# Optimization experiments

Measured on AMD Instinct MI355X. Metric: run time of the kernel, lower is better.

Reference implementation:

```python
import jax, jax.numpy as jnp
import numpy as np

B, N, N2 = 4, 4096, 4096
CIN, DIM, KNN, UP = 128, 64, 20, 2
HPOS, HATT = 64, 256
EPS = 1e-5


def _group(feat, idx):
    # feat: (B,C,M), idx: (B,N,K) -> (B,C,N,K) gather of neighbor features
    return jax.vmap(lambda f, i: f[:, i])(feat, idx)


def _conv1d(w, b, x):
    # 1x1 Conv1d: w (O,C), x (B,C,N)
    return jnp.einsum('oc,bcn->bon', w, x) + b[:, None]


def _bn(x, g, be, m, v):
    # eval-mode BatchNorm2d on (B,C,N,K)
    inv = g / jnp.sqrt(v + EPS)
    return x * inv[:, None, None] + (be - m * inv)[:, None, None]


def setup_inputs() -> dict:
    key = jax.random.key(0)
    ks = jax.random.split(key, 32)
    r = lambda i, s: jax.random.normal(ks[i], s, jnp.float32)
    u = lambda i, s: jax.random.uniform(ks[i], s, jnp.float32, 0.5, 1.5)
    return {
        'pos1': r(0, (B, 3, N)),
        'query': r(1, (B, CIN, N)),
        'pos2': r(2, (B, 3, N2)),
        'key_feat': r(3, (B, CIN, N2)),
        'wq': r(4, (DIM, CIN)) * 0.05, 'bq': r(5, (DIM,)) * 0.05,
        'wk': r(6, (DIM, CIN)) * 0.05, 'bk': r(7, (DIM,)) * 0.05,
        'wv': r(8, (DIM, CIN)) * 0.05, 'bv': r(9, (DIM,)) * 0.05,
        'pw1': r(10, (HPOS, 3)) * 0.2, 'pb1': r(11, (HPOS,)) * 0.05,
        'pg': u(12, (HPOS,)), 'pbt': r(13, (HPOS,)) * 0.05,
        'pm': r(14, (HPOS,)) * 0.05, 'pv': u(15, (HPOS,)),
        'pw2': r(16, (DIM, HPOS)) * 0.1, 'pb2': r(17, (DIM,)) * 0.05,
        'aw1': r(18, (HATT, DIM)) * 0.1, 'ab1': r(19, (HATT,)) * 0.05,
        'ag': u(20, (HATT,)), 'abt2': r(21, (HATT,)) * 0.05,
        'am': r(22, (HATT,)) * 0.05, 'av': u(23, (HATT,)),
        'awt': r(24, (HATT, DIM, UP)) * 0.05, 'abt': r(25, (DIM,)) * 0.05,
        'we': r(26, (CIN, DIM)) * 0.1, 'be': r(27, (CIN,)) * 0.05,
    }


def reference(pos1, query, pos2, key_feat, wq, bq, wk, bk, wv, bv,
              pw1, pb1, pg, pbt, pm, pv, pw2, pb2,
              aw1, ab1, ag, abt2, am, av, awt, abt, we, be):
    q = _conv1d(wq, bq, query)          # (B,DIM,N)
    k = _conv1d(wk, bk, key_feat)       # (B,DIM,N2)
    v = _conv1d(wv, bv, key_feat)       # (B,DIM,N2)
    # KNN of pos1 queries into pos2 support set
    p1 = pos1.transpose(0, 2, 1)        # (B,N,3)
    p2 = pos2.transpose(0, 2, 1)        # (B,N2,3)
    d = (jnp.sum(p1 * p1, -1)[:, :, None] + jnp.sum(p2 * p2, -1)[:, None, :]
         - 2.0 * jnp.einsum('bnd,bmd->bnm', p1, p2))
    _, idx = jax.lax.top_k(-d, KNN)     # (B,N,KNN)
    kg = _group(k, idx)                 # (B,DIM,N,K)
    qk_rel = q[:, :, :, None] - kg
    pos_rel = pos1[:, :, :, None] - _group(pos2, idx)   # (B,3,N,K)
    # pos_mlp: conv2d 3->HPOS, BN, ReLU, conv2d HPOS->DIM
    pe = jnp.einsum('oc,bcnk->bonk', pw1, pos_rel) + pb1[:, None, None]
    pe = jax.nn.relu(_bn(pe, pg, pbt, pm, pv))
    pe = jnp.einsum('oc,bcnk->bonk', pw2, pe) + pb2[:, None, None]  # (B,DIM,N,K)
    # attn_mlp: conv2d DIM->HATT, BN, ReLU, ConvTranspose2d HATT->DIM kernel (UP,1)
    h = qk_rel + pe
    a = jnp.einsum('oc,bcnk->bonk', aw1, h) + ab1[:, None, None]
    a = jax.nn.relu(_bn(a, ag, abt2, am, av))               # (B,HATT,N,K)
    att = jnp.einsum('bcnk,cor->bonrk', a, awt).reshape(B, DIM, N * UP, KNN)
    att = att + abt[:, None, None]
    att = jax.nn.softmax(att, axis=-1)
    vg = _group(v, idx) + pe            # (B,DIM,N,K)
    vu = jnp.repeat(vg, UP, axis=2)     # nearest upsample -> (B,DIM,N*UP,K)
    agg = jnp.sum(att * vu, axis=-1)    # (B,DIM,N*UP)
    y = _conv1d(we, be, agg)            # (B,CIN,N*UP)
    identity = jnp.repeat(query, UP, axis=2)  # residual (in==out -> Identity)
    return y + identity
```

## Files before the change

kernel.cpp:

```cpp
#include <hip/hip_runtime.h>
#include <hip/hip_bf16.h>

#define BATCH 4
#define NPTS  4096
#define NPTS2 4096
#define CIN   128
#define DIM   64
#define KNN   20
#define UPF   2
#define HPOS  64
#define HATT  256
#define MOUT  8192
#define EPSF  1e-5f
#define QPB   3
#define BPB   1366

#define FB_KNN   1024
#define FB_PKV   (FB_KNN + 256)
#define FB_PQ    (FB_PKV + 256)
#define FB_PACK  (FB_PQ + 128)

typedef _Float16 h16x8 __attribute__((ext_vector_type(8)));
typedef _Float16 h16x4 __attribute__((ext_vector_type(4)));
typedef _Float16 h16x2 __attribute__((ext_vector_type(2)));
typedef float    f32x4 __attribute__((ext_vector_type(4)));

__device__ inline float rdlane(float v, int src) {
  return __int_as_float(__builtin_amdgcn_readlane(__float_as_int(v), src));
}

__device__ __forceinline__ float distf(float qn, float m2x, float m2y, float m2z,
                                       float x, float y, float z) {
  float s = __fmaf_rn(x, x, qn);
  s = __fmaf_rn(y, y, s);
  s = __fmaf_rn(z, z, s);
  s = __fmaf_rn(m2x, x, s);
  s = __fmaf_rn(m2y, y, s);
  s = __fmaf_rn(m2z, z, s);
  return s;
}

__global__ __launch_bounds__(256) void front(
    const float* __restrict__ pos1, const float* __restrict__ pos2,
    int* __restrict__ idxout,
    const float* __restrict__ key_feat,
    const float* __restrict__ wk, const float* __restrict__ bk,
    const float* __restrict__ wv, const float* __restrict__ bv,
    float* __restrict__ k_t, float* __restrict__ v_t,
    const float* __restrict__ query,
    const float* __restrict__ wq, const float* __restrict__ bq,
    float* __restrict__ q_t,
    const float* __restrict__ aw1, const float* __restrict__ awt,
    const float* __restrict__ pw2,
    const float* __restrict__ ag,  const float* __restrict__ av,
    const float* __restrict__ abt2, const float* __restrict__ am,
    const float* __restrict__ abt,
    const float* __restrict__ pg,  const float* __restrict__ pv,
    const float* __restrict__ pbt, const float* __restrict__ pm,
    const float* __restrict__ ab1, const float* __restrict__ pb1,
    const float* __restrict__ pw1,
    _Float16* __restrict__ aw1h, _Float16* __restrict__ awtP,
    _Float16* __restrict__ pw2h, float* __restrict__ abtX,
    float* __restrict__ ab1f, float* __restrict__ pw1f,
    float* __restrict__ pb1f) {
  __shared__ union {
    struct { float X[CIN][64]; float O[64][65]; } pj;
    struct { int cnt[16]; float dbuf[16][64]; int jbuf[16][64]; } kn;
  } smU;
  const int bid = blockIdx.x;
  const int t   = threadIdx.x;

  if (bid < FB_KNN) {
    const int lane = t & 63;
    const int wv   = t >> 6;
    const int b    = bid >> 8;
    const int nb   = (bid & 255) * 16;
    const float* p2x = pos2 + (b * 3 + 0) * NPTS2;
    const float* p2y = pos2 + (b * 3 + 1) * NPTS2;
    const float* p2z = pos2 + (b * 3 + 2) * NPTS2;

    float qn[4], m2x[4], m2y[4], m2z[4];
#pragma unroll
    for (int qi = 0; qi < 4; ++qi) {
      int n = nb + wv * 4 + qi;
      float qx = pos1[(b * 3 + 0) * NPTS + n];
      float qy = pos1[(b * 3 + 1) * NPTS + n];
      float qz = pos1[(b * 3 + 2) * NPTS + n];
      qn[qi]  = qx * qx + qy * qy + qz * qz;
      m2x[qi] = -2.0f * qx; m2y[qi] = -2.0f * qy; m2z[qi] = -2.0f * qz;
    }

    float mymin[4] = {3.402823466e38f, 3.402823466e38f,
                      3.402823466e38f, 3.402823466e38f};
    f32x4 cx[4], cy[4], cz[4];
#pragma unroll 1
    for (int c = 0; c < 4; ++c) {
      int base = c * 1024 + lane * 4;
#pragma unroll
      for (int g = 0; g < 4; ++g) {
        cx[g] = *(const f32x4*)(p2x + base + g * 256);
        cy[g] = *(const f32x4*)(p2y + base + g * 256);
        cz[g] = *(const f32x4*)(p2z + base + g * 256);
      }
#pragma unroll
      for (int qi = 0; qi < 4; ++qi)
#pragma unroll
        for (int g = 0; g < 4; ++g)
#pragma unroll
          for (int e = 0; e < 4; ++e) {
            float d = distf(qn[qi], m2x[qi], m2y[qi], m2z[qi],
                            cx[g][e], cy[g][e], cz[g][e]);
            mymin[qi] = fminf(mymin[qi], d);
          }
    }

    float T0[4];
#pragma unroll
    for (int qi = 0; qi < 4; ++qi) {
      float v = mymin[qi];
#pragma unroll
      for (int k = 2; k <= 64; k <<= 1)
#pragma unroll
        for (int jj = k >> 1; jj >= 1; jj >>= 1) {
          float o = __shfl_xor(v, jj);
          bool up = ((lane & k) == 0);
          bool keepmin = (((lane & jj) == 0) == up);
          v = keepmin ? fminf(v, o) : fmaxf(v, o);
        }
      T0[qi] = rdlane(v, 19);
    }

    if (lane < 4) smU.kn.cnt[wv * 4 + lane] = 0;

#pragma unroll 1
    for (int c = 0; c < 4; ++c) {
      int base = c * 1024 + lane * 4;
#pragma unroll
      for (int g = 0; g < 4; ++g) {
        cx[g] = *(const f32x4*)(p2x + base + g * 256);
        cy[g] = *(const f32x4*)(p2y + base + g * 256);
        cz[g] = *(const f32x4*)(p2z + base + g * 256);
      }
#pragma unroll
      for (int qi = 0; qi < 4; ++qi) {
        const int qq = wv * 4 + qi;
#pragma unroll
        for (int g = 0; g < 4; ++g)
#pragma unroll
          for (int e = 0; e < 4; ++e) {
            float d = distf(qn[qi], m2x[qi], m2y[qi], m2z[qi],
                            cx[g][e], cy[g][e], cz[g][e]);
            if (d <= T0[qi]) {
              int slot = atomicAdd(&smU.kn.cnt[qq], 1);
              if (slot < 64) { smU.kn.dbuf[qq][slot] = d; smU.kn.jbuf[qq][slot] = base + g * 256 + e; }
            }
          }
      }
    }

#pragma unroll 1
    for (int qi = 0; qi < 4; ++qi) {
      const int qq = wv * 4 + qi;
      const int n  = nb + qq;
      const int cnt = smU.kn.cnt[qq];
      if (cnt <= 64) {
        float dk = (lane < cnt) ? smU.kn.dbuf[qq][lane] : 3.402823466e38f;
        int   jk = (lane < cnt) ? smU.kn.jbuf[qq][lane] : 0x7fffffff;
#pragma unroll
        for (int k = 2; k <= 64; k <<= 1) {
#pragma unroll
          for (int jj = k >> 1; jj >= 1; jj >>= 1) {
            float od = __shfl_xor(dk, jj);
            int   oj = __shfl_xor(jk, jj);
            bool mineSm = (dk < od) || (dk == od && jk < oj);
            bool up = ((lane & k) == 0);
            bool keepmin = (((lane & jj) == 0) == up);
            bool takeOther = (keepmin != mineSm);
            dk = takeOther ? od : dk;
            jk = takeOther ? oj : jk;
          }
        }
        if (lane < KNN) idxout[(b * NPTS + n) * KNN + lane] = jk;
      } else {
        float dl = 3.402823466e38f;
        int   il = 0;
        for (int j0 = 0; j0 < NPTS2; j0 += 64) {
          int j = j0 + lane;
          float d = distf(qn[qi], m2x[qi], m2y[qi], m2z[qi], p2x[j], p2y[j], p2z[j]);
          float T = rdlane(dl, 19);
          unsigned long long m = __ballot(d < T);
          while (m) {
            int src = __ffsll(m) - 1;
            m &= m - 1;
            float dd = rdlane(d, src);
            float T2 = rdlane(dl, 19);
            if (dd < T2) {
              int jj2 = j0 + src;
              float pd = __shfl_up(dl, 1);
              int   pi = __shfl_up(il, 1);
              if (dl > dd) {
                if (lane == 0 || pd <= dd) { dl = dd; il = jj2; }
                else                       { dl = pd; il = pi; }
              }
            }
          }
        }
        if (lane < KNN) idxout[(b * NPTS + n) * KNN + lane] = il;
      }
    }
  } else if (bid < FB_PKV) {
    const int vb = bid - FB_KNN;
    const int b  = vb >> 6;
    const int n0 = (vb & 63) * 64;
    for (int l = t; l < CIN * 64; l += 256) {
      int c = l >> 6, i = l & 63;
      smU.pj.X[c][i] = key_feat[(b * CIN + c) * NPTS2 + n0 + i];
    }
    __syncthreads();
    const int n_l = t & 63;
    const int w   = __builtin_amdgcn_readfirstlane(t >> 6);
    float acck[16], accv[16];
#pragma unroll
    for (int i = 0; i < 16; ++i) { acck[i] = bk[w * 16 + i]; accv[i] = bv[w * 16 + i]; }
    for (int c = 0; c < CIN; ++c) {
      float xv = smU.pj.X[c][n_l];
#pragma unroll
      for (int i = 0; i < 16; ++i) {
        acck[i] += wk[(w * 16 + i) * CIN + c] * xv;
        accv[i] += wv[(w * 16 + i) * CIN + c] * xv;
      }
    }
#pragma unroll
    for (int i = 0; i < 16; ++i) smU.pj.O[n_l][w * 16 + i] = acck[i];
    __syncthreads();
    for (int l = t; l < 64 * 64; l += 256)
      k_t[(b * NPTS2 + n0 + (l >> 6)) * DIM + (l & 63)] = smU.pj.O[l >> 6][l & 63];
    __syncthreads();
#pragma unroll
    for (int i = 0; i < 16; ++i) smU.pj.O[n_l][w * 16 + i] = accv[i];
    __syncthreads();
    for (int l = t; l < 64 * 64; l += 256)
      v_t[(b * NPTS2 + n0 + (l >> 6)) * DIM + (l & 63)] = smU.pj.O[l >> 6][l & 63];
  } else if (bid < FB_PQ) {
    const int vb = bid - FB_PKV;
    const int b  = vb >> 6;
    const int n0 = (vb & 63) * 64;
    for (int l = t; l < CIN * 64; l += 256) {
      int c = l >> 6, i = l & 63;
      smU.pj.X[c][i] = query[(b * CIN + c) * NPTS + n0 + i];
    }
    __syncthreads();
    const int n_l = t & 63;
    const int w   = __builtin_amdgcn_readfirstlane(t >> 6);
    float acc[16];
#pragma unroll
    for (int i = 0; i < 16; ++i) acc[i] = bq[w * 16 + i];
    for (int c = 0; c < CIN; ++c) {
      float xv = smU.pj.X[c][n_l];
#pragma unroll
      for (int i = 0; i < 16; ++i) acc[i] += wq[(w * 16 + i) * CIN + c] * xv;
    }
#pragma unroll
    for (int i = 0; i < 16; ++i) smU.pj.O[n_l][w * 16 + i] = acc[i];
    __syncthreads();
    for (int l = t; l < 64 * 64; l += 256)
      q_t[(b * NPTS + n0 + (l >> 6)) * DIM + (l & 63)] = smU.pj.O[l >> 6][l & 63];
  } else {
    int i = (bid - FB_PQ) * 256 + t;
    if (i < 16384) {
      int j = i >> 6;
      float inv = ag[j] / sqrtf(av[j] + EPSF);
      aw1h[i] = (_Float16)(aw1[i] * inv);
    }
    if (i < 32768) {
      int orr = i >> 8, j = i & 255;
      awtP[i] = (_Float16)awt[j * 128 + orr];
    }
    if (i < 4096) pw2h[i] = (_Float16)pw2[i];
    if (i < 256) {
      float inv = ag[i] / sqrtf(av[i] + EPSF);
      ab1f[i] = ab1[i] * inv + (abt2[i] - am[i] * inv);
    }
    if (i < 192) {
      int hc = i / 3;
      float inv = pg[hc] / sqrtf(pv[hc] + EPSF);
      pw1f[i] = pw1[i] * inv;
    }
    if (i < 128) abtX[i] = abt[i >> 1];
    if (i < 64) {
      float inv = pg[i] / sqrtf(pv[i] + EPSF);
      pb1f[i] = pb1[i] * inv + (pbt[i] - pm[i] * inv);
    }
  }
}

#define SM_R0    0
#define SM_R1    9216
#define SM_LGC   0
#define SM_VGB   18432

__global__ __launch_bounds__(256, 4) void attn_mfma(
    const float* __restrict__ q_t, const float* __restrict__ k_t,
    const float* __restrict__ v_t, const int* __restrict__ idx,
    const float* __restrict__ pos1, const float* __restrict__ pos2,
    const float* __restrict__ pw1f, const float* __restrict__ pb1f,
    const _Float16* __restrict__ pw2h, const float* __restrict__ pb2,
    const _Float16* __restrict__ aw1h, const float* __restrict__ ab1f,
    const _Float16* __restrict__ awtP, const float* __restrict__ abtX,
    float* __restrict__ agg) {
  __shared__ __align__(16) char smem[27136];
  const int b  = blockIdx.x / BPB;
  const int n0 = (blockIdx.x - b * BPB) * QPB;
  const int t  = threadIdx.x;
  const int lane = t & 63;
  const int w  = t >> 6;
  const int r  = lane & 15;
  const int q4 = lane >> 4;

  const int colB = t & 63, cgB = t >> 6;
  const int pB = colB / 20, kkB = colB - pB * 20;
  const bool okB = (pB < QPB) && (n0 + pB < NPTS);
  const int nqB = okB ? (n0 + pB) : 0;
  int jB = 0;
  if (okB) jB = idx[(b * NPTS + nqB) * KNN + kkB];

  f32x4 qk4[4], vv4[4];
  {
    const float* qrow = q_t + ((size_t)(b * NPTS  + nqB)) * DIM + cgB * 16;
    const float* krow = k_t + ((size_t)(b * NPTS2 + jB))  * DIM + cgB * 16;
    const float* vrow = v_t + ((size_t)(b * NPTS2 + jB))  * DIM + cgB * 16;
#pragma unroll
    for (int u = 0; u < 4; ++u) {
      f32x4 qv = *(const f32x4*)(qrow + u * 4);
      f32x4 kv = *(const f32x4*)(krow + u * 4);
      qk4[u] = qv - kv;
      vv4[u] = *(const f32x4*)(vrow + u * 4);
    }
  }

  {
    float p0 = 0.f, p1 = 0.f, p2 = 0.f;
    if (okB) {
      p0 = pos1[(b * 3 + 0) * NPTS + nqB] - pos2[(b * 3 + 0) * NPTS2 + jB];
      p1 = pos1[(b * 3 + 1) * NPTS + nqB] - pos2[(b * 3 + 1) * NPTS2 + jB];
      p2 = pos1[(b * 3 + 2) * NPTS + nqB] - pos2[(b * 3 + 2) * NPTS2 + jB];
    }
#pragma unroll
    for (int hf = 0; hf < 2; ++hf) {
      h16x8 pk;
#pragma unroll
      for (int ii = 0; ii < 8; ++ii) {
        int hc = cgB * 16 + hf * 8 + ii;
        float v0 = pb1f[hc] + pw1f[hc*3] * p0 + pw1f[hc*3+1] * p1 + pw1f[hc*3+2] * p2;
        v0 = fmaxf(v0, 0.f);
        if (!okB) v0 = 0.f;
        pk[ii] = (_Float16)v0;
      }
      *(h16x8*)(smem + SM_R0 + ((colB * 72 + cgB * 16 + hf * 8) * 2)) = pk;
    }
  }
  __syncthreads();

  {
    h16x8 a0[2];
#pragma unroll
    for (int ks = 0; ks < 2; ++ks)
      a0[ks] = *(const h16x8*)&pw2h[(w * 16 + r) * 64 + ks * 32 + q4 * 8];
    f32x4 acc[4];
#pragma unroll
    for (int nt = 0; nt < 4; ++nt) acc[nt] = (f32x4){0.f, 0.f, 0.f, 0.f};
#pragma unroll
    for (int ks = 0; ks < 2; ++ks)
#pragma unroll
      for (int nt = 0; nt < 4; ++nt) {
        h16x8 bv = *(h16x8*)(smem + SM_R0 + ((nt * 16 + r) * 72 + ks * 32 + q4 * 8) * 2);
        acc[nt] = __builtin_amdgcn_mfma_f32_16x16x32_f16(a0[ks], bv, acc[nt], 0, 0, 0);
      }
    int o0 = w * 16 + q4 * 4;
    f32x4 pbv = *(const f32x4*)&pb2[o0];
#pragma unroll
    for (int nt = 0; nt < 4; ++nt) {
      f32x4 vv = acc[nt] + pbv;
      h16x4 pk = {(_Float16)vv[0], (_Float16)vv[1], (_Float16)vv[2], (_Float16)vv[3]};
      *(h16x4*)(smem + SM_R1 + ((nt * 16 + r) * 72 + o0) * 2) = pk;
    }
  }

  {
    h16x8 pe8[2];
#pragma unroll
    for (int hf = 0; hf < 2; ++hf)
      pe8[hf] = *(h16x8*)(smem + SM_R1 + (colB * 72 + cgB * 16 + hf * 8) * 2);
    h16x8 hp8[2];
#pragma unroll
    for (int u = 0; u < 4; ++u) {
      int hf = u >> 1, e0 = (u & 1) * 4;
      f32x4 pe = {(float)pe8[hf][e0],     (float)pe8[hf][e0 + 1],
                  (float)pe8[hf][e0 + 2], (float)pe8[hf][e0 + 3]};
      f32x4 hv = qk4[u] + pe;
      f32x4 gv = vv4[u] + pe;
      if (!okB) { hv = (f32x4){0.f,0.f,0.f,0.f}; gv = hv; }
      hp8[hf][e0]     = (_Float16)hv[0];
      hp8[hf][e0 + 1] = (_Float16)hv[1];
      hp8[hf][e0 + 2] = (_Float16)hv[2];
      hp8[hf][e0 + 3] = (_Float16)hv[3];
      h16x4 gp = {(_Float16)gv[0], (_Float16)gv[1], (_Float16)gv[2], (_Float16)gv[3]};
      *(h16x4*)(smem + SM_VGB + (colB * 68 + cgB * 16 + u * 4) * 2) = gp;
    }
#pragma unroll
    for (int hf = 0; hf < 2; ++hf)
      *(h16x8*)(smem + SM_R1 + (colB * 72 + cgB * 16 + hf * 8) * 2) = hp8[hf];
  }
  __syncthreads();

  h16x8 bs[2][4];
#pragma unroll
  for (int ks = 0; ks < 2; ++ks)
#pragma unroll
    for (int nt = 0; nt < 4; ++nt)
      bs[ks][nt] = *(h16x8*)(smem + SM_R1 + ((nt * 16 + r) * 72 + ks * 32 + q4 * 8) * 2);

  f32x4 accD[2][4];
#pragma unroll
  for (int h = 0; h < 2; ++h)
#pragma unroll
    for (int nt = 0; nt < 4; ++nt) accD[h][nt] = (f32x4){0.f, 0.f, 0.f, 0.f};

#define C_QUARTER(quar, base)                                                  \
  {                                                                            \
    int mt = (quar) * 4 + w;                                                   \
    h16x8 af0 = *(const h16x8*)&aw1h[(mt * 16 + r) * 64 + q4 * 8];             \
    h16x8 af1 = *(const h16x8*)&aw1h[(mt * 16 + r) * 64 + 32 + q4 * 8];        \
    f32x4 acc[4];                                                              \
    _Pragma("unroll")                                                          \
    for (int nt = 0; nt < 4; ++nt) acc[nt] = (f32x4){0.f, 0.f, 0.f, 0.f};      \
    _Pragma("unroll")                                                          \
    for (int nt = 0; nt < 4; ++nt)                                             \
      acc[nt] = __builtin_amdgcn_mfma_f32_16x16x32_f16(af0, bs[0][nt], acc[nt], 0, 0, 0); \
    _Pragma("unroll")                                                          \
    for (int nt = 0; nt < 4; ++nt)                                             \
      acc[nt] = __builtin_amdgcn_mfma_f32_16x16x32_f16(af1, bs[1][nt], acc[nt], 0, 0, 0); \
    int j0  = mt * 16 + q4 * 4;                                                \
    int jq0 = j0 - (quar) * 64;                                                \
    f32x4 b1 = *(const f32x4*)&ab1f[j0];                                       \
    _Pragma("unroll")                                                          \
    for (int nt = 0; nt < 4; ++nt) {                                           \
      int col = nt * 16 + r;                                                   \
      float v0 = fmaxf(acc[nt][0] + b1[0], 0.f);                               \
      float v1 = fmaxf(acc[nt][1] + b1[1], 0.f);                               \
      float v2 = fmaxf(acc[nt][2] + b1[2], 0.f);                               \
      float v3 = fmaxf(acc[nt][3] + b1[3], 0.f);                               \
      h16x4 pk = {(_Float16)v0, (_Float16)v1, (_Float16)v2, (_Float16)v3};     \
      *(h16x4*)(smem + (base) + (col * 72 + jq0) * 2) = pk;                    \
    }                                                                          \
  }

#define D_QUARTER(quar, base)                                                  \
  {                                                                            \
    _Pragma("unroll")                                                          \
    for (int ks2 = 0; ks2 < 2; ++ks2) {                                        \
      h16x8 bsv[4];                                                            \
      _Pragma("unroll")                                                        \
      for (int nt = 0; nt < 4; ++nt)                                           \
        bsv[nt] = *(h16x8*)(smem + (base) + ((nt * 16 + r) * 72 + ks2 * 32 + q4 * 8) * 2); \
      int ksg = (quar) * 2 + ks2;                                              \
      _Pragma("unroll")                                                        \
      for (int h = 0; h < 2; ++h) {                                            \
        int mt2 = w * 2 + h;                                                   \
        h16x8 af = *(const h16x8*)&awtP[(mt2 * 16 + r) * 256 + ksg * 32 + q4 * 8]; \
        _Pragma("unroll")                                                      \
        for (int nt = 0; nt < 4; ++nt)                                         \
          accD[h][nt] = __builtin_amdgcn_mfma_f32_16x16x32_f16(af, bsv[nt], accD[h][nt], 0, 0, 0); \
      }                                                                        \
    }                                                                          \
  }

  C_QUARTER(0, SM_R0)
  __syncthreads();
  D_QUARTER(0, SM_R0)
  C_QUARTER(1, SM_R1)
  __syncthreads();
  D_QUARTER(1, SM_R1)
  C_QUARTER(2, SM_R0)
  __syncthreads();
  D_QUARTER(2, SM_R0)
  C_QUARTER(3, SM_R1)
  __syncthreads();
  D_QUARTER(3, SM_R1)
  __syncthreads();

  {
#pragma unroll
    for (int h = 0; h < 2; ++h) {
      int orr0 = (w * 2 + h) * 16 + q4 * 4;
      f32x4 ab = *(const f32x4*)&abtX[orr0];
#pragma unroll
      for (int nt = 0; nt < 4; ++nt) {
        int col = nt * 16 + r;
        if (col < QPB * KNN) {
          f32x4 vv = accD[h][nt] + ab;
          h16x4 pk = {(_Float16)vv[0], (_Float16)vv[1], (_Float16)vv[2], (_Float16)vv[3]};
          *(h16x4*)(smem + SM_LGC + (col * 136 + orr0) * 2) = pk;
        }
      }
    }
  }
  __syncthreads();

  if (t < 64 * QPB) {
    int li = t & 63, p = t >> 6;
    if (n0 + p < NPTS) {
      h16x2 Lp[KNN];
      float G[KNN];
#pragma unroll
      for (int kk = 0; kk < KNN; ++kk) {
        Lp[kk] = *(h16x2*)(smem + SM_LGC + ((p * 20 + kk) * 136 + li * 2) * 2);
        G[kk]  = (float)*(_Float16*)(smem + SM_VGB + ((p * 20 + kk) * 68 + li) * 2);
      }
#pragma unroll
      for (int half = 0; half < 2; ++half) {
        float mx = (float)Lp[0][half];
#pragma unroll
        for (int kk = 1; kk < KNN; ++kk) mx = fmaxf(mx, (float)Lp[kk][half]);
        float s = 0.f, a = 0.f;
#pragma unroll
        for (int kk = 0; kk < KNN; ++kk) {
          float e = __expf((float)Lp[kk][half] - mx);
          s += e;
          a += e * G[kk];
        }
        float rs = 1.0f / s;
        agg[(((size_t)(b * NPTS + n0 + p)) * UPF + half) * DIM + li] = a * rs;
      }
    }
  }
#undef C_QUARTER
#undef D_QUARTER
}

__global__ __launch_bounds__(256) void out_proj(const float* __restrict__ agg,
    const float* __restrict__ we, const float* __restrict__ be,
    const float* __restrict__ query, float* __restrict__ out) {
  __shared__ float A[64][65];
  const int b  = blockIdx.x >> 7;
  const int m0 = (blockIdx.x & 127) * 64;
  const int t  = threadIdx.x;
  for (int l = t; l < 64 * 64; l += 256) {
    int row = l >> 6, c = l & 63;
    A[row][c] = agg[(b * MOUT + m0 + row) * DIM + c];
  }
  __syncthreads();
  const int m_l = t & 63;
  const int w   = __builtin_amdgcn_readfirstlane(t >> 6);
  float acc[32];
#pragma unroll
  for (int i = 0; i < 32; ++i) acc[i] = 0.f;
  for (int c = 0; c < DIM; ++c) {
    float a = A[m_l][c];
#pragma unroll
    for (int i = 0; i < 32; ++i) acc[i] += we[(w * 32 + i) * DIM + c] * a;
  }
  const int m = m0 + m_l;
#pragma unroll
  for (int i = 0; i < 32; ++i) {
    int o = w * 32 + i;
    out[(b * CIN + o) * MOUT + m] = acc[i] + be[o] + query[(b * CIN + o) * NPTS + (m >> 1)];
  }
}

extern "C" void kernel_launch(void* const* d_in, const int* in_sizes, int n_in,
                              void* d_out, int out_size, void* d_ws, size_t ws_size,
                              hipStream_t stream) {
  (void)in_sizes; (void)n_in; (void)out_size; (void)ws_size;
  const float* pos1     = (const float*)d_in[0];
  const float* query    = (const float*)d_in[1];
  const float* pos2     = (const float*)d_in[2];
  const float* key_feat = (const float*)d_in[3];
  const float* wq  = (const float*)d_in[4];
  const float* bq  = (const float*)d_in[5];
  const float* wk  = (const float*)d_in[6];
  const float* bk  = (const float*)d_in[7];
  const float* wv  = (const float*)d_in[8];
  const float* bv  = (const float*)d_in[9];
  const float* pw1 = (const float*)d_in[10];
  const float* pb1 = (const float*)d_in[11];
  const float* pg  = (const float*)d_in[12];
  const float* pbt = (const float*)d_in[13];
  const float* pm  = (const float*)d_in[14];
  const float* pv  = (const float*)d_in[15];
  const float* pw2 = (const float*)d_in[16];
  const float* pb2 = (const float*)d_in[17];
  const float* aw1 = (const float*)d_in[18];
  const float* ab1 = (const float*)d_in[19];
  const float* ag  = (const float*)d_in[20];
  const float* abt2= (const float*)d_in[21];
  const float* am  = (const float*)d_in[22];
  const float* av  = (const float*)d_in[23];
  const float* awt = (const float*)d_in[24];
  const float* abt = (const float*)d_in[25];
  const float* we  = (const float*)d_in[26];
  const float* be  = (const float*)d_in[27];

  float* ws   = (float*)d_ws;
  float* q_t  = ws;
  float* k_t  = q_t + BATCH * NPTS * DIM;
  float* v_t  = k_t + BATCH * NPTS2 * DIM;
  float* aggb = v_t + BATCH * NPTS2 * DIM;
  int*   idxb = (int*)(aggb + BATCH * MOUT * DIM);
  _Float16* aw1h = (_Float16*)(idxb + BATCH * NPTS * KNN);
  _Float16* awtP = aw1h + HATT * DIM;
  _Float16* pw2h = awtP + 128 * HATT;
  float* abtX    = (float*)(pw2h + DIM * HPOS);
  float* ab1f    = abtX + 128;
  float* pw1f    = ab1f + HATT;
  float* pb1f    = pw1f + HPOS * 3;

  front<<<FB_PACK, 256, 0, stream>>>(
      pos1, pos2, idxb,
      key_feat, wk, bk, wv, bv, k_t, v_t,
      query, wq, bq, q_t,
      aw1, awt, pw2, ag, av, abt2, am, abt,
      pg, pv, pbt, pm, ab1, pb1, pw1,
      aw1h, awtP, pw2h, abtX, ab1f, pw1f, pb1f);
  attn_mfma<<<BATCH * BPB, 256, 0, stream>>>(q_t, k_t, v_t, idxb, pos1, pos2,
      pw1f, pb1f, pw2h, pb2, aw1h, ab1f, awtP, abtX, aggb);
  out_proj<<<BATCH * (MOUT / 64), 256, 0, stream>>>(aggb, we, be, query, (float*)d_out);
}
```

Before: 318.4 us.

## Cut register pressure in attention MFMA kernel to raise occupancy to 5 blocks

Stops keeping the B fragments of the hidden tile and the preloaded A fragments in registers; they are now reloaded from shared memory inside each K-step. The C/D quarter stages drop the SM_R0/SM_R1 ping-pong, since SM_R1 now holds the persistent input, and use a single buffer with an extra barrier between stages. Launch bounds go from 4 to 5 blocks per SIMD-group so more waves can be resident. The trade is more LDS reads and twice the barriers in exchange for lower VGPR use and higher occupancy.

```diff
diff --git a/kernel.cpp b/kernel.cpp
--- a/kernel.cpp
+++ b/kernel.cpp
@@ -299,7 +299,7 @@
 #define SM_LGC   0
 #define SM_VGB   18432
 
-__global__ __launch_bounds__(256, 4) void attn_mfma(
+__global__ __launch_bounds__(256, 5) void attn_mfma(
     const float* __restrict__ q_t, const float* __restrict__ k_t,
     const float* __restrict__ v_t, const int* __restrict__ idx,
     const float* __restrict__ pos1, const float* __restrict__ pos2,
@@ -362,20 +362,18 @@
   __syncthreads();
 
   {
-    h16x8 a0[2];
-#pragma unroll
-    for (int ks = 0; ks < 2; ++ks)
-      a0[ks] = *(const h16x8*)&pw2h[(w * 16 + r) * 64 + ks * 32 + q4 * 8];
     f32x4 acc[4];
 #pragma unroll
     for (int nt = 0; nt < 4; ++nt) acc[nt] = (f32x4){0.f, 0.f, 0.f, 0.f};
 #pragma unroll
-    for (int ks = 0; ks < 2; ++ks)
+    for (int ks = 0; ks < 2; ++ks) {
+      h16x8 a0 = *(const h16x8*)&pw2h[(w * 16 + r) * 64 + ks * 32 + q4 * 8];
 #pragma unroll
       for (int nt = 0; nt < 4; ++nt) {
         h16x8 bv = *(h16x8*)(smem + SM_R0 + ((nt * 16 + r) * 72 + ks * 32 + q4 * 8) * 2);
-        acc[nt] = __builtin_amdgcn_mfma_f32_16x16x32_f16(a0[ks], bv, acc[nt], 0, 0, 0);
-      }
+        acc[nt] = __builtin_amdgcn_mfma_f32_16x16x32_f16(a0, bv, acc[nt], 0, 0, 0);
+      }
+    }
     int o0 = w * 16 + q4 * 4;
     f32x4 pbv = *(const f32x4*)&pb2[o0];
 #pragma unroll
@@ -413,33 +411,29 @@
   }
   __syncthreads();
 
-  h16x8 bs[2][4];
-#pragma unroll
-  for (int ks = 0; ks < 2; ++ks)
-#pragma unroll
-    for (int nt = 0; nt < 4; ++nt)
-      bs[ks][nt] = *(h16x8*)(smem + SM_R1 + ((nt * 16 + r) * 72 + ks * 32 + q4 * 8) * 2);
-
   f32x4 accD[2][4];
 #pragma unroll
   for (int h = 0; h < 2; ++h)
 #pragma unroll
     for (int nt = 0; nt < 4; ++nt) accD[h][nt] = (f32x4){0.f, 0.f, 0.f, 0.f};
 
-#define C_QUARTER(quar, base)                                                  \
+#define C_QUARTER(quar)                                                        \
   {                                                                            \
     int mt = (quar) * 4 + w;                                                   \
-    h16x8 af0 = *(const h16x8*)&aw1h[(mt * 16 + r) * 64 + q4 * 8];             \
-    h16x8 af1 = *(const h16x8*)&aw1h[(mt * 16 + r) * 64 + 32 + q4 * 8];        \
     f32x4 acc[4];                                                              \
     _Pragma("unroll")                                                          \
     for (int nt = 0; nt < 4; ++nt) acc[nt] = (f32x4){0.f, 0.f, 0.f, 0.f};      \
     _Pragma("unroll")                                                          \
-    for (int nt = 0; nt < 4; ++nt)                                             \
-      acc[nt] = __builtin_amdgcn_mfma_f32_16x16x32_f16(af0, bs[0][nt], acc[nt], 0, 0, 0); \
-    _Pragma("unroll")                                                          \
-    for (int nt = 0; nt < 4; ++nt)                                             \
-      acc[nt] = __builtin_amdgcn_mfma_f32_16x16x32_f16(af1, bs[1][nt], acc[nt], 0, 0, 0); \
+    for (int ks = 0; ks < 2; ++ks) {                                           \
+      h16x8 af = *(const h16x8*)&aw1h[(mt * 16 + r) * 64 + ks * 32 + q4 * 8];  \
+      h16x8 bsv[4];                                                            \
+      _Pragma("unroll")                                                        \
+      for (int nt = 0; nt < 4; ++nt)                                           \
+        bsv[nt] = *(h16x8*)(smem + SM_R1 + ((nt * 16 + r) * 72 + ks * 32 + q4 * 8) * 2); \
+      _Pragma("unroll")                                                        \
+      for (int nt = 0; nt < 4; ++nt)                                           \
+        acc[nt] = __builtin_amdgcn_mfma_f32_16x16x32_f16(af, bsv[nt], acc[nt], 0, 0, 0); \
+    }                                                                          \
     int j0  = mt * 16 + q4 * 4;                                                \
     int jq0 = j0 - (quar) * 64;                                                \
     f32x4 b1 = *(const f32x4*)&ab1f[j0];                                       \
@@ -451,18 +445,18 @@
       float v2 = fmaxf(acc[nt][2] + b1[2], 0.f);                               \
       float v3 = fmaxf(acc[nt][3] + b1[3], 0.f);                               \
       h16x4 pk = {(_Float16)v0, (_Float16)v1, (_Float16)v2, (_Float16)v3};     \
-      *(h16x4*)(smem + (base) + (col * 72 + jq0) * 2) = pk;                    \
+      *(h16x4*)(smem + SM_R0 + (col * 72 + jq0) * 2) = pk;                     \
     }                                                                          \
   }
 
-#define D_QUARTER(quar, base)                                                  \
+#define D_QUARTER(quar)                                                        \
   {                                                                            \
     _Pragma("unroll")                                                          \
     for (int ks2 = 0; ks2 < 2; ++ks2) {                                        \
       h16x8 bsv[4];                                                            \
       _Pragma("unroll")                                                        \
       for (int nt = 0; nt < 4; ++nt)                                           \
-        bsv[nt] = *(h16x8*)(smem + (base) + ((nt * 16 + r) * 72 + ks2 * 32 + q4 * 8) * 2); \
+        bsv[nt] = *(h16x8*)(smem + SM_R0 + ((nt * 16 + r) * 72 + ks2 * 32 + q4 * 8) * 2); \
       int ksg = (quar) * 2 + ks2;                                              \
       _Pragma("unroll")                                                        \
       for (int h = 0; h < 2; ++h) {                                            \
@@ -475,18 +469,21 @@
     }                                                                          \
   }
 
-  C_QUARTER(0, SM_R0)
-  __syncthreads();
-  D_QUARTER(0, SM_R0)
-  C_QUARTER(1, SM_R1)
-  __syncthreads();
-  D_QUARTER(1, SM_R1)
-  C_QUARTER(2, SM_R0)
-  __syncthreads();
-  D_QUARTER(2, SM_R0)
-  C_QUARTER(3, SM_R1)
-  __syncthreads();
-  D_QUARTER(3, SM_R1)
+  C_QUARTER(0)
+  __syncthreads();
+  D_QUARTER(0)
+  __syncthreads();
+  C_QUARTER(1)
+  __syncthreads();
+  D_QUARTER(1)
+  __syncthreads();
+  C_QUARTER(2)
+  __syncthreads();
+  D_QUARTER(2)
+  __syncthreads();
+  C_QUARTER(3)
+  __syncthreads();
+  D_QUARTER(3)
   __syncthreads();
 
   {
```

Measured after the change: 325.6 us. +2.2%, slower.
